# Optimization experiments

Measured on AMD Instinct MI355X. Metric: run time of the kernel, lower is better.

Reference implementation:

```python
import jax, jax.numpy as jnp
import numpy as np

D, DFFN, H, P, L = 256, 1024, 8, 4, 4
B, LQ = 32, 300
LENS = [2048, 1024, 512, 256]
STARTS = [0, 2048, 3072, 3584]
S = sum(LENS)


def setup_inputs() -> dict:
    key = jax.random.key(0)
    ks = iter(jax.random.split(key, 64))
    def W(shape, s=0.02):
        return jax.random.normal(next(ks), shape, jnp.float32) * s
    inp = {}
    inp['tgt'] = W((B, LQ, D), 1.0)
    inp['query_pos'] = W((B, LQ, D), 1.0)
    centers = jax.random.uniform(next(ks), (B, LQ, L))
    widths = 0.05 + 0.2 * jax.random.uniform(next(ks), (B, LQ, L))
    inp['reference_points'] = jnp.stack([centers, widths], -1)  # (B,Lq,L,2) = (center,width)
    inp['src'] = W((B, S, D), 1.0)
    inp['temporal_lengths'] = np.array(LENS, np.int64)
    inp['level_start_index'] = np.array(STARTS, np.int64)
    for n, shape in [('sa_qw', (D, D)), ('sa_kw', (D, D)), ('sa_vw', (D, D)), ('sa_ow', (D, D)), ('ff1_w', (D, DFFN)), ('ff2_w', (DFFN, D))]:
        inp[n] = W(shape)
    for n, sz in [('sa_qb', D), ('sa_kb', D), ('sa_vb', D), ('sa_ob', D), ('ff1_b', DFFN), ('ff2_b', D)]:
        inp[n] = jnp.zeros((sz,), jnp.float32)
    for pre in ['ca', 'se']:
        inp[pre + '_off_w'] = W((D, H * L * P))
        inp[pre + '_off_b'] = jnp.zeros((H * L * P,), jnp.float32)
        inp[pre + '_attn_w'] = W((D, H * L * P))
        inp[pre + '_attn_b'] = jnp.zeros((H * L * P,), jnp.float32)
        inp[pre + '_val_w'] = W((D, D))
        inp[pre + '_val_b'] = jnp.zeros((D,), jnp.float32)
        inp[pre + '_out_w'] = W((D, D))
        inp[pre + '_out_b'] = jnp.zeros((D,), jnp.float32)
    for n in ['ln1', 'lnse', 'ln2', 'ln3']:
        inp[n + '_g'] = jnp.ones((D,), jnp.float32)
        inp[n + '_b'] = jnp.zeros((D,), jnp.float32)
    return inp


def _ln(x, g, b, eps=1e-5):
    m = jnp.mean(x, -1, keepdims=True)
    v = jnp.mean((x - m) ** 2, -1, keepdims=True)
    return (x - m) * jax.lax.rsqrt(v + eps) * g + b


def _mha(q, k, v, qw, qb, kw, kb, vw, vb, ow, ob):
    b, lq, d = q.shape
    dh = d // H
    qh = (q @ qw + qb).reshape(b, lq, H, dh).transpose(0, 2, 1, 3)
    kh = (k @ kw + kb).reshape(b, -1, H, dh).transpose(0, 2, 1, 3)
    vh = (v @ vw + vb).reshape(b, -1, H, dh).transpose(0, 2, 1, 3)
    scores = jnp.einsum('bhqd,bhkd->bhqk', qh, kh) * (dh ** -0.5)
    attn = jax.nn.softmax(scores, -1)
    out = jnp.einsum('bhqk,bhkd->bhqd', attn, vh).transpose(0, 2, 1, 3).reshape(b, lq, d)
    return out @ ow + ob


def _deform(q, ref, src, lens, starts, vw, vb, offw, offb, aw, ab, ow, ob, boundary):
    b, lq, d = q.shape
    dh = d // H
    value = (src @ vw + vb).reshape(b, -1, H, dh)  # (B,S,H,Dh)
    off = (q @ offw + offb).reshape(b, lq, H, L, P)
    attn = jax.nn.softmax((q @ aw + ab).reshape(b, lq, H, L * P), -1).reshape(b, lq, H, L, P)
    center = ref[..., 0][:, :, None, :, None]  # (B,Lq,1,L,1)
    width = ref[..., 1][:, :, None, :, None]
    if boundary:
        # half the points anchored at segment start, half at segment end
        sign = jnp.where(jnp.arange(P) < P // 2, -0.5, 0.5)
        anchor = center + sign * width
    else:
        anchor = center
    loc = anchor + off / P * width * 0.5  # normalized sampling locations (B,Lq,H,L,P)
    out = jnp.zeros((b, lq, H, dh), value.dtype)
    for l in range(L):
        T = int(lens[l]); s0 = int(starts[l])
        v = value[:, s0:s0 + T].transpose(0, 2, 1, 3)  # (B,H,T,Dh)
        x = loc[:, :, :, l, :] * T - 0.5  # align_corners=False grid
        x0 = jnp.floor(x)
        w = x - x0
        i0 = x0.astype(jnp.int32)
        i1 = i0 + 1
        m0 = ((i0 >= 0) & (i0 < T)).astype(v.dtype)
        m1 = ((i1 >= 0) & (i1 < T)).astype(v.dtype)
        i0c = jnp.clip(i0, 0, T - 1)
        i1c = jnp.clip(i1, 0, T - 1)
        def gather(idx):
            idxh = idx.transpose(0, 2, 1, 3).reshape(b, H, lq * P, 1)
            g = jnp.take_along_axis(v, jnp.broadcast_to(idxh, (b, H, lq * P, dh)), axis=2)
            return g.reshape(b, H, lq, P, dh).transpose(0, 2, 1, 3, 4)  # (B,Lq,H,P,Dh)
        samp = gather(i0c) * ((1 - w) * m0)[..., None] + gather(i1c) * (w * m1)[..., None]
        out = out + jnp.einsum('bqhp,bqhpd->bqhd', attn[:, :, :, l, :], samp)
    return out.reshape(b, lq, d) @ ow + ob


def reference(tgt, query_pos, reference_points, src, temporal_lengths, level_start_index,
              sa_qw, sa_qb, sa_kw, sa_kb, sa_vw, sa_vb, sa_ow, sa_ob,
              ca_off_w, ca_off_b, ca_attn_w, ca_attn_b, ca_val_w, ca_val_b, ca_out_w, ca_out_b,
              se_off_w, se_off_b, se_attn_w, se_attn_b, se_val_w, se_val_b, se_out_w, se_out_b,
              ff1_w, ff1_b, ff2_w, ff2_b,
              ln1_g, ln1_b, lnse_g, lnse_b, ln2_g, ln2_b, ln3_g, ln3_b):
    lens = np.asarray(temporal_lengths)
    starts = np.asarray(level_start_index)
    q = tgt + query_pos
    t2 = _mha(q, q, tgt, sa_qw, sa_qb, sa_kw, sa_kb, sa_vw, sa_vb, sa_ow, sa_ob)
    tgt = _ln(tgt + t2, ln2_g, ln2_b)
    t2 = _deform(tgt + query_pos, reference_points, src, lens, starts,
                 ca_val_w, ca_val_b, ca_off_w, ca_off_b, ca_attn_w, ca_attn_b, ca_out_w, ca_out_b, False)
    tgt = _ln(tgt + t2, ln1_g, ln1_b)
    t2 = _deform(tgt + query_pos, reference_points, src, lens, starts,
                 se_val_w, se_val_b, se_off_w, se_off_b, se_attn_w, se_attn_b, se_out_w, se_out_b, True)
    tgt = _ln(tgt + t2, lnse_g, lnse_b)
    t2 = jax.nn.relu(tgt @ ff1_w + ff1_b) @ ff2_w + ff2_b
    tgt = _ln(tgt + t2, ln3_g, ln3_b)
    return tgt
```

## Files before the change

kernel.cpp:

```cpp
#include <hip/hip_runtime.h>
#include <hip/hip_bf16.h>

namespace {

typedef unsigned short u16;
typedef unsigned int u32;

constexpr int D    = 256;
constexpr int H    = 8;
constexpr int DH   = 32;
constexpr int B    = 32;
constexpr int LQ   = 300;
constexpr int NQ   = B * LQ;
constexpr int S    = 3840;
constexpr int MS   = B * S;
constexpr int DFFN = 1024;

typedef __attribute__((ext_vector_type(8))) short bf16x8;
typedef __attribute__((ext_vector_type(4))) float f32x4;

__device__ inline u16 f2b(float x) {
  u32 u = __builtin_bit_cast(u32, x);
  u32 r = (u + 0x7FFFu + ((u >> 16) & 1u)) >> 16;
  return (u16)r;
}
__device__ inline u32 pk2(float a, float b) {
  return (u32)f2b(a) | ((u32)f2b(b) << 16);
}
__device__ inline void unpack2(u32 w, float& a, float& b) {
  a = __builtin_bit_cast(float, w << 16);
  b = __builtin_bit_cast(float, w & 0xffff0000u);
}

__global__ __launch_bounds__(256) void gemm_qkv(
    const u16* __restrict__ qbuf, const u16* __restrict__ tgtb,
    const u16* __restrict__ saqk_t, const u16* __restrict__ sav_t,
    const float* __restrict__ qkb, const float* __restrict__ vbias,
    u16* __restrict__ qkbuf, u16* __restrict__ vh)
{
  constexpr int K = 256, BK = 64, LDK = 72;
  __shared__ __align__(16) u16 sh[128 * LDK];
  u16* As = sh;
  u16* Bs = sh + 64 * LDK;
  const bool isv = blockIdx.x >= 8;
  const u16* A  = isv ? tgtb : qbuf;
  const u16* Bt = isv ? sav_t : saqk_t;
  const float* bias = isv ? vbias : qkb;
  u16* C = isv ? vh : qkbuf;
  const int N = isv ? 256 : 512;
  const int n0 = (isv ? (int)blockIdx.x - 8 : (int)blockIdx.x) * 64;
  const int m0 = blockIdx.y * 64;

  const int tid  = threadIdx.x;
  const int lane = tid & 63;
  const int wid  = tid >> 6;
  const int wm = wid >> 1, wn = wid & 1;

  f32x4 acc[2][2] = {};
  uint4 ra[2], rb[2];
  const int srow = tid >> 3, sch = (tid & 7) * 8;

#pragma unroll
  for (int i = 0; i < 2; ++i) {
    const int row = srow + i * 32;
    ra[i] = *(const uint4*)(A  + (size_t)(m0 + row) * K + sch);
    rb[i] = *(const uint4*)(Bt + (size_t)(n0 + row) * K + sch);
  }
  for (int t = 0; t < 4; ++t) {
#pragma unroll
    for (int i = 0; i < 2; ++i) {
      const int row = srow + i * 32;
      *(uint4*)(&As[row * LDK + sch]) = ra[i];
      *(uint4*)(&Bs[row * LDK + sch]) = rb[i];
    }
    __syncthreads();
    if (t + 1 < 4) {
      const int k0 = (t + 1) * BK;
#pragma unroll
      for (int i = 0; i < 2; ++i) {
        const int row = srow + i * 32;
        ra[i] = *(const uint4*)(A  + (size_t)(m0 + row) * K + k0 + sch);
        rb[i] = *(const uint4*)(Bt + (size_t)(n0 + row) * K + k0 + sch);
      }
    }
#pragma unroll
    for (int kk = 0; kk < 2; ++kk) {
      const int krd = kk * 32 + (lane >> 4) * 8;
      bf16x8 af[2], bf[2];
#pragma unroll
      for (int m = 0; m < 2; ++m)
        af[m] = *(const bf16x8*)(&As[(wm * 32 + (lane & 15) + 16 * m) * LDK + krd]);
#pragma unroll
      for (int n = 0; n < 2; ++n)
        bf[n] = *(const bf16x8*)(&Bs[(wn * 32 + (lane & 15) + 16 * n) * LDK + krd]);
#pragma unroll
      for (int m = 0; m < 2; ++m)
#pragma unroll
        for (int n = 0; n < 2; ++n)
          acc[m][n] = __builtin_amdgcn_mfma_f32_16x16x32_bf16(af[m], bf[n], acc[m][n], 0, 0, 0);
    }
    __syncthreads();
  }

  const int cr = (lane >> 4) * 4;
  const int cc = lane & 15;
  u16* stg = sh;
#pragma unroll
  for (int n = 0; n < 2; ++n) {
    const int lc = wn * 32 + n * 16 + cc;
    const float bv = bias[n0 + lc];
#pragma unroll
    for (int m = 0; m < 2; ++m) {
      const int lr0 = wm * 32 + m * 16 + cr;
#pragma unroll
      for (int r = 0; r < 4; ++r)
        stg[(lr0 + r) * LDK + lc] = f2b(acc[m][n][r] + bv);
    }
  }
  __syncthreads();
#pragma unroll
  for (int i = 0; i < 2; ++i) {
    const int c = tid + 256 * i;
    const int row = c >> 3, ch = c & 7;
    *(uint4*)(C + (size_t)(m0 + row) * N + n0 + ch * 8) =
        *(const uint4*)(&stg[row * LDK + ch * 8]);
  }
}

__global__ __launch_bounds__(512) void gemm_val4(
    const float* __restrict__ A, const u16* __restrict__ Bt2,
    const float* __restrict__ bias2, u16* __restrict__ Vca, u16* __restrict__ Vse)
{
  __shared__ __align__(16) char shraw[33792];
  char* Asw = shraw;
  const int tid  = threadIdx.x;
  const int lane = tid & 63;
  const int w    = tid >> 6;
  const int bid  = blockIdx.x;
  const int nh   = (bid >> 3) & 1;
  const int m0   = ((bid >> 4) * 8 + (bid & 7)) * 64;
  u16* dst = nh ? Vse : Vca;
  const u16* Bt = Bt2 + nh * 256 * 256;
  const float* bias = bias2 + nh * 256;
  const int b  = m0 / S;
  const int s0 = m0 - b * S;

#pragma unroll
  for (int i = 0; i < 4; ++i) {
    const int idx = tid + 512 * i;
    const int row = idx >> 5, ch = idx & 31;
    const float* ap = A + (size_t)(m0 + row) * 256 + ch * 8;
    const float4 f0 = *(const float4*)(ap);
    const float4 f1 = *(const float4*)(ap + 4);
    uint4 pk;
    pk.x = pk2(f0.x, f0.y); pk.y = pk2(f0.z, f0.w);
    pk.z = pk2(f1.x, f1.y); pk.w = pk2(f1.z, f1.w);
    *(uint4*)(Asw + row * 512 + ((ch * 16) ^ ((row & 7) << 4))) = pk;
  }
  __syncthreads();

  f32x4 acc[4][2] = {};
  const u16* bb = Bt + (size_t)(w * 32 + (lane & 15)) * 256 + (lane >> 4) * 8;
  bf16x8 bcur[2], bnxt[2];
#pragma unroll
  for (int n = 0; n < 2; ++n) bcur[n] = *(const bf16x8*)(bb + n * 4096);

#pragma unroll
  for (int kk = 0; kk < 8; ++kk) {
    bf16x8 af[4];
    const int kb = kk * 64 + (lane >> 4) * 16;
#pragma unroll
    for (int m = 0; m < 4; ++m) {
      const int row = m * 16 + (lane & 15);
      af[m] = *(const bf16x8*)(Asw + row * 512 + (kb ^ ((row & 7) << 4)));
    }
    if (kk < 7) {
#pragma unroll
      for (int n = 0; n < 2; ++n)
        bnxt[n] = *(const bf16x8*)(bb + n * 4096 + (kk + 1) * 32);
    }
#pragma unroll
    for (int m = 0; m < 4; ++m)
#pragma unroll
      for (int n = 0; n < 2; ++n)
        acc[m][n] = __builtin_amdgcn_mfma_f32_16x16x32_bf16(af[m], bcur[n], acc[m][n], 0, 0, 0);
#pragma unroll
    for (int n = 0; n < 2; ++n) bcur[n] = bnxt[n];
  }
  __syncthreads();

  constexpr int STC = 264;
  u16* stg = (u16*)shraw;
  const int cr = (lane >> 4) * 4;
  const int cc = lane & 15;
#pragma unroll
  for (int n = 0; n < 2; ++n) {
    const int col = w * 32 + n * 16 + cc;
    const float bv = bias[col];
#pragma unroll
    for (int m = 0; m < 4; ++m) {
      const int r0 = m * 16 + cr;
#pragma unroll
      for (int r = 0; r < 4; ++r)
        stg[(r0 + r) * STC + col] = f2b(acc[m][n][r] + bv);
    }
  }
  __syncthreads();
  u16* vb = dst + (size_t)b * H * S * DH;
#pragma unroll
  for (int i = 0; i < 4; ++i) {
    const int c = tid + 512 * i;
    const int row = c >> 5, ch = c & 31;
    const int h = ch >> 2, dq = ch & 3;
    *(uint4*)(vb + ((size_t)h * S + (s0 + row)) * DH + dq * 8) =
        *(const uint4*)(&stg[row * STC + ch * 8]);
  }
}

__global__ __launch_bounds__(1024) void gemm_lnoff(
    const u16* __restrict__ A, const u16* __restrict__ Bt,
    const float* __restrict__ bias, const float* __restrict__ res,
    const float* __restrict__ g, const float* __restrict__ be,
    const float* __restrict__ qpos,
    const u16* __restrict__ offw, const float* __restrict__ offb,
    float* __restrict__ fout, float* __restrict__ oaout)
{
  constexpr int K = 256, LDK = 72;
  __shared__ __align__(16) float ftile[64 * 264];
  u16* As = (u16*)ftile;
  u16* Bs = As + 64 * LDK;
  u16* aq = (u16*)ftile;
  const int tid  = threadIdx.x;
  const int lane = tid & 63;
  const int wid  = tid >> 6;
  const int wm = wid >> 2, wn = wid & 3;
  const int m0 = blockIdx.x * 64;

  f32x4 acc[4] = {};
  const bool am = tid < 512;
  const int arow = tid >> 3, ach = (tid & 7) * 8;

  uint4 ra = {};
  uint4 rb[2];
  if (am) ra = *(const uint4*)(A + (size_t)(m0 + arow) * K + ach);
#pragma unroll
  for (int i = 0; i < 2; ++i) {
    const int idx = tid + 1024 * i;
    const int brow = idx >> 3, bch = (idx & 7) * 8;
    rb[i] = *(const uint4*)(Bt + (size_t)brow * K + bch);
  }

  for (int t = 0; t < 4; ++t) {
    if (am) *(uint4*)(&As[arow * LDK + ach]) = ra;
#pragma unroll
    for (int i = 0; i < 2; ++i) {
      const int idx = tid + 1024 * i;
      const int brow = idx >> 3, bch = (idx & 7) * 8;
      *(uint4*)(&Bs[brow * LDK + bch]) = rb[i];
    }
    __syncthreads();
    if (t + 1 < 4) {
      const int k0 = (t + 1) * 64;
      if (am) ra = *(const uint4*)(A + (size_t)(m0 + arow) * K + k0 + ach);
#pragma unroll
      for (int i = 0; i < 2; ++i) {
        const int idx = tid + 1024 * i;
        const int brow = idx >> 3, bch = (idx & 7) * 8;
        rb[i] = *(const uint4*)(Bt + (size_t)brow * K + k0 + bch);
      }
    }
#pragma unroll
    for (int kk = 0; kk < 2; ++kk) {
      const int krd = kk * 32 + (lane >> 4) * 8;
      bf16x8 af, bf[4];
      af = *(const bf16x8*)(&As[(wm * 16 + (lane & 15)) * LDK + krd]);
#pragma unroll
      for (int n = 0; n < 4; ++n)
        bf[n] = *(const bf16x8*)(&Bs[(wn * 64 + n * 16 + (lane & 15)) * LDK + krd]);
#pragma unroll
      for (int n = 0; n < 4; ++n)
        acc[n] = __builtin_amdgcn_mfma_f32_16x16x32_bf16(af, bf[n], acc[n], 0, 0, 0);
    }
    __syncthreads();
  }

  const int cr = (lane >> 4) * 4;
  const int cc = lane & 15;
#pragma unroll
  for (int n = 0; n < 4; ++n) {
    const int col = wn * 64 + n * 16 + cc;
    const float bv = bias[col];
#pragma unroll
    for (int r = 0; r < 4; ++r)
      ftile[(wm * 16 + cr + r) * 264 + col] = acc[n][r] + bv;
  }
  __syncthreads();

  const int row = tid >> 4, s16 = tid & 15;
  const size_t grow = (size_t)(m0 + row) * 256;
  float vv[16];
  float sum = 0.f;
#pragma unroll
  for (int j = 0; j < 4; ++j) {
    const int col = s16 * 4 + j * 64;
    const float4 fv = *(const float4*)(&ftile[row * 264 + col]);
    const float4 rv = *(const float4*)(res + grow + col);
    vv[j * 4 + 0] = fv.x + rv.x; vv[j * 4 + 1] = fv.y + rv.y;
    vv[j * 4 + 2] = fv.z + rv.z; vv[j * 4 + 3] = fv.w + rv.w;
    sum += vv[j * 4 + 0] + vv[j * 4 + 1] + vv[j * 4 + 2] + vv[j * 4 + 3];
  }
  sum += __shfl_xor(sum, 1, 64);
  sum += __shfl_xor(sum, 2, 64);
  sum += __shfl_xor(sum, 4, 64);
  sum += __shfl_xor(sum, 8, 64);
  const float mean = sum * (1.f / 256.f);
  float sq = 0.f;
#pragma unroll
  for (int k = 0; k < 16; ++k) { const float d = vv[k] - mean; sq += d * d; }
  sq += __shfl_xor(sq, 1, 64);
  sq += __shfl_xor(sq, 2, 64);
  sq += __shfl_xor(sq, 4, 64);
  sq += __shfl_xor(sq, 8, 64);
  const float rstd = rsqrtf(sq * (1.f / 256.f) + 1e-5f);

  float yq[16];
#pragma unroll
  for (int j = 0; j < 4; ++j) {
    const int col = s16 * 4 + j * 64;
    const float4 gv = *(const float4*)(g + col);
    const float4 bv = *(const float4*)(be + col);
    const float4 qv = *(const float4*)(qpos + grow + col);
    float4 y;
    y.x = (vv[j * 4 + 0] - mean) * rstd * gv.x + bv.x;
    y.y = (vv[j * 4 + 1] - mean) * rstd * gv.y + bv.y;
    y.z = (vv[j * 4 + 2] - mean) * rstd * gv.z + bv.z;
    y.w = (vv[j * 4 + 3] - mean) * rstd * gv.w + bv.w;
    *(float4*)(fout + grow + col) = y;
    yq[j * 4 + 0] = y.x + qv.x; yq[j * 4 + 1] = y.y + qv.y;
    yq[j * 4 + 2] = y.z + qv.z; yq[j * 4 + 3] = y.w + qv.w;
  }
  __syncthreads();

#pragma unroll
  for (int j = 0; j < 4; ++j) {
    const int col = s16 * 4 + j * 64;
    uint2 pk;
    pk.x = pk2(yq[j * 4 + 0], yq[j * 4 + 1]);
    pk.y = pk2(yq[j * 4 + 2], yq[j * 4 + 3]);
    *(uint2*)(&aq[row * 264 + col]) = pk;
  }
  __syncthreads();

  f32x4 acc2[4] = {};
  const u16* bb = offw + (size_t)(wn * 64 + (lane & 15)) * 256 + (lane >> 4) * 8;
#pragma unroll
  for (int kk = 0; kk < 8; ++kk) {
    const bf16x8 af = *(const bf16x8*)(&aq[(wm * 16 + (lane & 15)) * 264 + kk * 32 + (lane >> 4) * 8]);
#pragma unroll
    for (int n = 0; n < 4; ++n) {
      const bf16x8 bf = *(const bf16x8*)(bb + (size_t)n * 16 * 256 + kk * 32);
      acc2[n] = __builtin_amdgcn_mfma_f32_16x16x32_bf16(af, bf, acc2[n], 0, 0, 0);
    }
  }
  __syncthreads();

#pragma unroll
  for (int n = 0; n < 4; ++n) {
    const int col = wn * 64 + n * 16 + cc;
    const float bv = offb[col];
#pragma unroll
    for (int r = 0; r < 4; ++r)
      ftile[(wm * 16 + cr + r) * 264 + col] = acc2[n][r] + bv;
  }
  __syncthreads();
#pragma unroll
  for (int i = 0; i < 4; ++i) {
    const int c = tid + 1024 * i;
    const int rw = c >> 6, ch = c & 63;
    *(float4*)(oaout + (size_t)(m0 + rw) * 256 + ch * 4) =
        *(const float4*)(&ftile[rw * 264 + ch * 4]);
  }
}

__global__ __launch_bounds__(512) void gemm_tail(
    const u16* __restrict__ A, const u16* __restrict__ Wout,
    const float* __restrict__ bout, const float* __restrict__ res,
    const float* __restrict__ g1, const float* __restrict__ be1,
    const u16* __restrict__ B1t, const u16* __restrict__ B2t,
    const float* __restrict__ b1, const float* __restrict__ b2,
    const float* __restrict__ g2, const float* __restrict__ be2,
    float* __restrict__ fout)
{
  __shared__ __align__(16) char sh[81920];
  char* Ast = sh;
  char* ffh = sh + 16384;
  float* ftile = (float*)sh;
  const int tid  = threadIdx.x;
  const int lane = tid & 63;
  const int w    = tid >> 6;
  const int m0   = blockIdx.x * 32;
  const int cr = (lane >> 4) * 4;
  const int cc = lane & 15;

#pragma unroll
  for (int i = 0; i < 2; ++i) {
    const int idx = tid + 512 * i;
    const int row = idx >> 5, ch = idx & 31;
    const uint4 v = *(const uint4*)(A + (size_t)(m0 + row) * 256 + ch * 8);
    *(uint4*)(Ast + row * 512 + ((ch * 16) ^ ((row & 7) << 4))) = v;
  }
  __syncthreads();

  f32x4 accB[2][2] = {};
  {
    const u16* bb = Wout + (size_t)(w * 32 + (lane & 15)) * 256 + (lane >> 4) * 8;
#pragma unroll
    for (int kk = 0; kk < 8; ++kk) {
      bf16x8 af[2];
      const int kb = kk * 64 + (lane >> 4) * 16;
#pragma unroll
      for (int m = 0; m < 2; ++m) {
        const int row = m * 16 + (lane & 15);
        af[m] = *(const bf16x8*)(Ast + row * 512 + (kb ^ ((row & 7) << 4)));
      }
#pragma unroll
      for (int n = 0; n < 2; ++n) {
        const bf16x8 bf = *(const bf16x8*)(bb + (size_t)n * 16 * 256 + kk * 32);
#pragma unroll
        for (int m = 0; m < 2; ++m)
          accB[m][n] = __builtin_amdgcn_mfma_f32_16x16x32_bf16(af[m], bf, accB[m][n], 0, 0, 0);
      }
    }
  }
  __syncthreads();

#pragma unroll
  for (int n = 0; n < 2; ++n) {
    const int col = w * 32 + n * 16 + cc;
    const float bv = bout[col];
#pragma unroll
    for (int m = 0; m < 2; ++m)
#pragma unroll
      for (int r = 0; r < 4; ++r)
        ftile[(m * 16 + cr + r) * 264 + col] = accB[m][n][r] + bv;
  }
  __syncthreads();

  const int row = tid >> 4, s16 = tid & 15;
  const size_t grow = (size_t)(m0 + row) * 256;
  float yv[16];
  {
    float vv[16];
    float sum = 0.f;
#pragma unroll
    for (int j = 0; j < 4; ++j) {
      const int col = s16 * 4 + j * 64;
      const float4 fv = *(const float4*)(&ftile[row * 264 + col]);
      const float4 rv = *(const float4*)(res + grow + col);
      vv[j * 4 + 0] = fv.x + rv.x; vv[j * 4 + 1] = fv.y + rv.y;
      vv[j * 4 + 2] = fv.z + rv.z; vv[j * 4 + 3] = fv.w + rv.w;
      sum += vv[j * 4 + 0] + vv[j * 4 + 1] + vv[j * 4 + 2] + vv[j * 4 + 3];
    }
    sum += __shfl_xor(sum, 1, 64);
    sum += __shfl_xor(sum, 2, 64);
    sum += __shfl_xor(sum, 4, 64);
    sum += __shfl_xor(sum, 8, 64);
    const float mean = sum * (1.f / 256.f);
    float sq = 0.f;
#pragma unroll
    for (int k = 0; k < 16; ++k) { const float d = vv[k] - mean; sq += d * d; }
    sq += __shfl_xor(sq, 1, 64);
    sq += __shfl_xor(sq, 2, 64);
    sq += __shfl_xor(sq, 4, 64);
    sq += __shfl_xor(sq, 8, 64);
    const float rstd = rsqrtf(sq * (1.f / 256.f) + 1e-5f);
#pragma unroll
    for (int j = 0; j < 4; ++j) {
      const int col = s16 * 4 + j * 64;
      const float4 gv = *(const float4*)(g1 + col);
      const float4 bv = *(const float4*)(be1 + col);
      yv[j * 4 + 0] = (vv[j * 4 + 0] - mean) * rstd * gv.x + bv.x;
      yv[j * 4 + 1] = (vv[j * 4 + 1] - mean) * rstd * gv.y + bv.y;
      yv[j * 4 + 2] = (vv[j * 4 + 2] - mean) * rstd * gv.z + bv.z;
      yv[j * 4 + 3] = (vv[j * 4 + 3] - mean) * rstd * gv.w + bv.w;
    }
  }
  __syncthreads();

#pragma unroll
  for (int j = 0; j < 4; ++j) {
    const int col = s16 * 4 + j * 64;
    uint2 pk;
    pk.x = pk2(yv[j * 4 + 0], yv[j * 4 + 1]);
    pk.y = pk2(yv[j * 4 + 2], yv[j * 4 + 3]);
    *(uint2*)(Ast + row * 512 + ((col * 2) ^ ((row & 7) << 4))) = pk;
  }
  __syncthreads();

  {
    f32x4 acc[2][8] = {};
    const u16* bb = B1t + (size_t)(w * 128 + (lane & 15)) * 256 + (lane >> 4) * 8;
#pragma unroll
    for (int kk = 0; kk < 8; ++kk) {
      bf16x8 af[2];
      const int kb = kk * 64 + (lane >> 4) * 16;
#pragma unroll
      for (int m = 0; m < 2; ++m) {
        const int rw = m * 16 + (lane & 15);
        af[m] = *(const bf16x8*)(Ast + rw * 512 + (kb ^ ((rw & 7) << 4)));
      }
#pragma unroll
      for (int n = 0; n < 8; ++n) {
        const bf16x8 bf = *(const bf16x8*)(bb + (size_t)n * 16 * 256 + kk * 32);
#pragma unroll
        for (int m = 0; m < 2; ++m)
          acc[m][n] = __builtin_amdgcn_mfma_f32_16x16x32_bf16(af[m], bf, acc[m][n], 0, 0, 0);
      }
    }
#pragma unroll
    for (int n = 0; n < 8; ++n) {
      const int col = w * 128 + n * 16 + cc;
      const float bv = b1[col];
#pragma unroll
      for (int m = 0; m < 2; ++m) {
#pragma unroll
        for (int r = 0; r < 4; ++r) {
          const int rw = m * 16 + cr + r;
          const float x = fmaxf(acc[m][n][r] + bv, 0.f);
          *(u16*)(ffh + rw * 2048 + ((col * 2) ^ ((rw & 7) << 4))) = f2b(x);
        }
      }
    }
  }
  __syncthreads();

  f32x4 acc2[2][2] = {};
  {
    const u16* bb = B2t + (size_t)(w * 32 + (lane & 15)) * 1024 + (lane >> 4) * 8;
#pragma unroll 4
    for (int kk = 0; kk < 32; ++kk) {
      bf16x8 af[2];
      const int kb = kk * 64 + (lane >> 4) * 16;
#pragma unroll
      for (int m = 0; m < 2; ++m) {
        const int rw = m * 16 + (lane & 15);
        af[m] = *(const bf16x8*)(ffh + rw * 2048 + (kb ^ ((rw & 7) << 4)));
      }
#pragma unroll
      for (int n = 0; n < 2; ++n) {
        const bf16x8 bf = *(const bf16x8*)(bb + (size_t)n * 16 * 1024 + kk * 32);
#pragma unroll
        for (int m = 0; m < 2; ++m)
          acc2[m][n] = __builtin_amdgcn_mfma_f32_16x16x32_bf16(af[m], bf, acc2[m][n], 0, 0, 0);
      }
    }
  }
  __syncthreads();

#pragma unroll
  for (int n = 0; n < 2; ++n) {
    const int col = w * 32 + n * 16 + cc;
    const float bv = b2[col];
#pragma unroll
    for (int m = 0; m < 2; ++m)
#pragma unroll
      for (int r = 0; r < 4; ++r)
        ftile[(m * 16 + cr + r) * 264 + col] = acc2[m][n][r] + bv;
  }
  __syncthreads();

  {
    float vv[16];
    float sum = 0.f;
#pragma unroll
    for (int j = 0; j < 4; ++j) {
      const int col = s16 * 4 + j * 64;
      const float4 fv = *(const float4*)(&ftile[row * 264 + col]);
      vv[j * 4 + 0] = fv.x + yv[j * 4 + 0]; vv[j * 4 + 1] = fv.y + yv[j * 4 + 1];
      vv[j * 4 + 2] = fv.z + yv[j * 4 + 2]; vv[j * 4 + 3] = fv.w + yv[j * 4 + 3];
      sum += vv[j * 4 + 0] + vv[j * 4 + 1] + vv[j * 4 + 2] + vv[j * 4 + 3];
    }
    sum += __shfl_xor(sum, 1, 64);
    sum += __shfl_xor(sum, 2, 64);
    sum += __shfl_xor(sum, 4, 64);
    sum += __shfl_xor(sum, 8, 64);
    const float mean = sum * (1.f / 256.f);
    float sq = 0.f;
#pragma unroll
    for (int k = 0; k < 16; ++k) { const float d = vv[k] - mean; sq += d * d; }
    sq += __shfl_xor(sq, 1, 64);
    sq += __shfl_xor(sq, 2, 64);
    sq += __shfl_xor(sq, 4, 64);
    sq += __shfl_xor(sq, 8, 64);
    const float rstd = rsqrtf(sq * (1.f / 256.f) + 1e-5f);
#pragma unroll
    for (int j = 0; j < 4; ++j) {
      const int col = s16 * 4 + j * 64;
      const float4 gv = *(const float4*)(g2 + col);
      const float4 bv = *(const float4*)(be2 + col);
      float4 y;
      y.x = (vv[j * 4 + 0] - mean) * rstd * gv.x + bv.x;
      y.y = (vv[j * 4 + 1] - mean) * rstd * gv.y + bv.y;
      y.z = (vv[j * 4 + 2] - mean) * rstd * gv.z + bv.z;
      y.w = (vv[j * 4 + 3] - mean) * rstd * gv.w + bv.w;
      *(float4*)(fout + grow + col) = y;
    }
  }
}

struct WSpec { const float* w; u16* wt; int K, N, blk0; };
struct WPack { WSpec s[14]; };

struct PrepArgs {
  const float *ca_off_b, *ca_attn_b, *se_off_b, *se_attn_b;
  const float *sa_qb, *sa_kb, *ca_val_b, *se_val_b;
  float *bias4, *qkb, *valb;
  const float *tgt, *qpos;
  u16 *tgtb, *qbuf;
  int n4, nwt;
};

__global__ __launch_bounds__(256) void prep_all(WPack p, PrepArgs a) {
  __shared__ float tile[32][33];
  const int b = blockIdx.x;
  if (b < a.nwt) {
    int i = 0;
#pragma unroll
    for (int j = 1; j < 14; ++j) if (b >= p.s[j].blk0) i = j;
    const float* w = p.s[i].w;
    u16* wt = p.s[i].wt;
    const int K = p.s[i].K, N = p.s[i].N;
    const int lb = b - p.s[i].blk0;
    const int ntN = N >> 5;
    const int tk = lb / ntN, tn = lb - tk * ntN;
    const int r = threadIdx.x >> 5, c = threadIdx.x & 31;
#pragma unroll
    for (int j = 0; j < 4; ++j)
      tile[r + j * 8][c] = w[(size_t)(tk * 32 + r + j * 8) * N + tn * 32 + c];
    __syncthreads();
#pragma unroll
    for (int j = 0; j < 4; ++j)
      wt[(size_t)(tn * 32 + r + j * 8) * K + tk * 32 + c] = f2b(tile[c][r + j * 8]);
  } else if (b == a.nwt) {
#pragma unroll
    for (int u = 0; u < 2; ++u) {
      const int t = threadIdx.x + 256 * u;
      a.bias4[t] = t < 128 ? a.ca_off_b[t] : t < 256 ? a.ca_attn_b[t - 128]
                 : t < 384 ? a.se_off_b[t - 256] : a.se_attn_b[t - 384];
      a.qkb[t]  = t < 256 ? a.sa_qb[t] : a.sa_kb[t - 256];
      a.valb[t] = t < 256 ? a.ca_val_b[t] : a.se_val_b[t - 256];
    }
  } else {
    const int i = (b - a.nwt - 1) * 256 + threadIdx.x;
    if (i < a.n4) {
      const float4 t = ((const float4*)a.tgt)[i];
      const float4 q = ((const float4*)a.qpos)[i];
      uint2 x, y;
      x.x = pk2(t.x, t.y); x.y = pk2(t.z, t.w);
      y.x = pk2(t.x + q.x, t.y + q.y); y.y = pk2(t.z + q.z, t.w + q.w);
      ((uint2*)a.tgtb)[i] = x;
      ((uint2*)a.qbuf)[i] = y;
    }
  }
}

__global__ __launch_bounds__(512) void mha_v2(
    const u16* __restrict__ qk, const u16* __restrict__ vh,
    u16* __restrict__ out)
{
  __shared__ __align__(16) float Ks[8 * 300 * 4];
  __shared__ __align__(16) float Vs[8 * 300 * 4];
  const int bh  = blockIdx.x & 255;
  const int seg = blockIdx.x >> 8;
  const int b = bh >> 3, h = bh & 7;
  const u16* kbase = qk + (size_t)b * LQ * 512 + 256 + h * DH;
  const u16* vbase = vh + (size_t)b * LQ * D + h * DH;
  for (int e = threadIdx.x; e < 300 * 8; e += 512) {
    const int r = e >> 3, j = e & 7;
    float4 f;
    const uint2 kv = *(const uint2*)(kbase + (size_t)r * 512 + j * 4);
    unpack2(kv.x, f.x, f.y);
    unpack2(kv.y, f.z, f.w);
    *(float4*)(&Ks[(j * 300 + r) * 4]) = f;
    const uint2 vv = *(const uint2*)(vbase + (size_t)r * D + j * 4);
    unpack2(vv.x, f.x, f.y);
    unpack2(vv.y, f.z, f.w);
    *(float4*)(&Vs[(j * 300 + r) * 4]) = f;
  }
  __syncthreads();

  const int lane = threadIdx.x & 63;
  const int lq = (threadIdx.x >> 6) * 16 + (lane >> 2);
  const int kc = lane & 3;
  const int q = seg * 128 + lq;
  if (q >= LQ) return;

  const u16* qrow = qk + (size_t)(b * LQ + q) * 512 + h * DH;
  float qv[DH];
#pragma unroll
  for (int c4 = 0; c4 < 4; ++c4) {
    const uint4 u = *(const uint4*)(qrow + c4 * 8);
    unpack2(u.x, qv[c4 * 8 + 0], qv[c4 * 8 + 1]);
    unpack2(u.y, qv[c4 * 8 + 2], qv[c4 * 8 + 3]);
    unpack2(u.z, qv[c4 * 8 + 4], qv[c4 * 8 + 5]);
    unpack2(u.w, qv[c4 * 8 + 6], qv[c4 * 8 + 7]);
  }
#pragma unroll
  for (int d = 0; d < DH; ++d) qv[d] *= 0.17677669529663689f;

  float o[DH] = {};
  float ssum = 0.f;
  const float* kp = &Ks[kc * 75 * 4];
  const float* vp = &Vs[kc * 75 * 4];
  for (int i = 0; i < 75; ++i) {
    float s = 0.f;
#pragma unroll
    for (int j = 0; j < 8; ++j) {
      const float4 kf = *(const float4*)(kp + i * 4 + j * 1200);
      s += qv[j * 4 + 0] * kf.x + qv[j * 4 + 1] * kf.y
         + qv[j * 4 + 2] * kf.z + qv[j * 4 + 3] * kf.w;
    }
    const float p = __expf(s);
    ssum += p;
#pragma unroll
    for (int j = 0; j < 8; ++j) {
      const float4 vf = *(const float4*)(vp + i * 4 + j * 1200);
      o[j * 4 + 0] += p * vf.x; o[j * 4 + 1] += p * vf.y;
      o[j * 4 + 2] += p * vf.z; o[j * 4 + 3] += p * vf.w;
    }
  }

  ssum += __shfl_xor(ssum, 1, 64);
  ssum += __shfl_xor(ssum, 2, 64);
#pragma unroll
  for (int d = 0; d < DH; ++d) {
    o[d] += __shfl_xor(o[d], 1, 64);
    o[d] += __shfl_xor(o[d], 2, 64);
  }
  const float inv = 1.f / ssum;

  u16* orow = out + (size_t)(b * LQ + q) * D + h * DH;
#pragma unroll
  for (int c = 0; c < 4; ++c) {
    if (kc == c) {
      uint4 w;
      w.x = pk2(o[c * 8 + 0] * inv, o[c * 8 + 1] * inv);
      w.y = pk2(o[c * 8 + 2] * inv, o[c * 8 + 3] * inv);
      w.z = pk2(o[c * 8 + 4] * inv, o[c * 8 + 5] * inv);
      w.w = pk2(o[c * 8 + 6] * inv, o[c * 8 + 7] * inv);
      *(uint4*)(orow + c * 8) = w;
    }
  }
}

template<bool BOUNDARY>
__global__ __launch_bounds__(512) void deform_v4(
    const float* __restrict__ oa, const float* __restrict__ ref,
    const u16* __restrict__ value, u16* __restrict__ out)
{
  __shared__ __align__(16) uint4 owt[4][128];
  const int unit = threadIdx.x >> 7;
  const int bq = blockIdx.x * 4 + unit;
  const int b = bq / LQ;
  const int t = threadIdx.x & 127;
  const int h = t >> 4;
  const int l = (t >> 2) & 3;
  const int p = t & 3;

  const float off   = oa[(size_t)bq * 256 + t];
  const float logit = oa[(size_t)bq * 256 + 128 + t];
  const float center = ref[(size_t)bq * 8 + l * 2 + 0];
  const float width  = ref[(size_t)bq * 8 + l * 2 + 1];

  const float e = __expf(logit);
  float ssum = e;
  ssum += __shfl_xor(ssum, 1, 64);
  ssum += __shfl_xor(ssum, 2, 64);
  ssum += __shfl_xor(ssum, 4, 64);
  ssum += __shfl_xor(ssum, 8, 64);
  const float wa = e / ssum;

  const int T  = 2048 >> l;
  const int s0 = 4096 - (4096 >> l);
  float anchor = center;
  if (BOUNDARY) anchor += (p < 2 ? -0.5f : 0.5f) * width;
  const float loc = anchor + off * width * 0.125f;
  const float x = loc * (float)T - 0.5f;
  const float x0 = floorf(x);
  const float w = x - x0;
  const int i0 = (int)x0;
  const int i1 = i0 + 1;
  const float w0 = (i0 >= 0 && i0 < T) ? wa * (1.f - w) : 0.f;
  const float w1 = (i1 >= 0 && i1 < T) ? wa * w : 0.f;
  const int i0c = min(max(i0, 0), T - 1);
  const int i1c = min(max(i1, 0), T - 1);
  uint4 pack;
  pack.x = (u32)((h * S + s0 + i0c) * (DH * 2));
  pack.y = __builtin_bit_cast(u32, w0);
  pack.z = (u32)((h * S + s0 + i1c) * (DH * 2));
  pack.w = __builtin_bit_cast(u32, w1);
  owt[unit][t] = pack;
  __syncthreads();

  const int g  = t >> 4;
  const int ln = t & 15;
  const int qd = ln & 3;
  const int ts = ln >> 2;
  const char* vb = (const char*)(value + (size_t)b * H * S * DH) + qd * 16;
  float o[8] = {};
#pragma unroll
  for (int i = 0; i < 8; ++i) {
    const int rowidx = i * 4 + ts;
    const uint4 ow = owt[unit][g * 16 + (rowidx >> 1)];
    const u32 boff = (rowidx & 1) ? ow.z : ow.x;
    const float wt = __builtin_bit_cast(float, (rowidx & 1) ? ow.w : ow.y);
    const uint4 v = *(const uint4*)(vb + boff);
    float a0, a1;
    unpack2(v.x, a0, a1); o[0] += wt * a0; o[1] += wt * a1;
    unpack2(v.y, a0, a1); o[2] += wt * a0; o[3] += wt * a1;
    unpack2(v.z, a0, a1); o[4] += wt * a0; o[5] += wt * a1;
    unpack2(v.w, a0, a1); o[6] += wt * a0; o[7] += wt * a1;
  }
#pragma unroll
  for (int d = 0; d < 8; ++d) {
    o[d] += __shfl_xor(o[d], 4, 64);
    o[d] += __shfl_xor(o[d], 8, 64);
  }
  if (ts == 0) {
    uint4 wv;
    wv.x = pk2(o[0], o[1]); wv.y = pk2(o[2], o[3]);
    wv.z = pk2(o[4], o[5]); wv.w = pk2(o[6], o[7]);
    *(uint4*)(out + (size_t)bq * D + g * DH + qd * 8) = wv;
  }
}

}

extern "C" void kernel_launch(void* const* d_in, const int* in_sizes, int n_in,
                              void* d_out, int out_size, void* d_ws, size_t ws_size,
                              hipStream_t stream)
{
  const float* tgt   = (const float*)d_in[0];
  const float* qpos  = (const float*)d_in[1];
  const float* ref   = (const float*)d_in[2];
  const float* src   = (const float*)d_in[3];
  const float* sa_qw = (const float*)d_in[6];
  const float* sa_kw = (const float*)d_in[7];
  const float* sa_vw = (const float*)d_in[8];
  const float* sa_ow = (const float*)d_in[9];
  const float* ff1_w = (const float*)d_in[10];
  const float* ff2_w = (const float*)d_in[11];
  const float* sa_qb = (const float*)d_in[12];
  const float* sa_kb = (const float*)d_in[13];
  const float* sa_vb = (const float*)d_in[14];
  const float* sa_ob = (const float*)d_in[15];
  const float* ff1_b = (const float*)d_in[16];
  const float* ff2_b = (const float*)d_in[17];
  const float* ca_off_w  = (const float*)d_in[18];
  const float* ca_off_b  = (const float*)d_in[19];
  const float* ca_attn_w = (const float*)d_in[20];
  const float* ca_attn_b = (const float*)d_in[21];
  const float* ca_val_w  = (const float*)d_in[22];
  const float* ca_val_b  = (const float*)d_in[23];
  const float* ca_out_w  = (const float*)d_in[24];
  const float* ca_out_b  = (const float*)d_in[25];
  const float* se_off_w  = (const float*)d_in[26];
  const float* se_off_b  = (const float*)d_in[27];
  const float* se_attn_w = (const float*)d_in[28];
  const float* se_attn_b = (const float*)d_in[29];
  const float* se_val_w  = (const float*)d_in[30];
  const float* se_val_b  = (const float*)d_in[31];
  const float* se_out_w  = (const float*)d_in[32];
  const float* se_out_b  = (const float*)d_in[33];
  const float* ln1_g  = (const float*)d_in[34];
  const float* ln1_b  = (const float*)d_in[35];
  const float* lnse_g = (const float*)d_in[36];
  const float* lnse_b = (const float*)d_in[37];
  const float* ln2_g  = (const float*)d_in[38];
  const float* ln2_b  = (const float*)d_in[39];
  const float* ln3_g  = (const float*)d_in[40];
  const float* ln3_b  = (const float*)d_in[41];

  const size_t ND = (size_t)NQ * D;
  const size_t MD = (size_t)MS * D;

  char* base = (char*)d_ws;
  size_t off = 0;
  auto alloc = [&](size_t bytes) -> void* {
    void* p = base + off;
    off += (bytes + 255) & ~(size_t)255;
    return p;
  };
  u16*  Vca  = (u16*)alloc(MD * 2);
  u16*  Vse  = (u16*)alloc(MD * 2);
  u16*  qkbuf = (u16*)alloc((size_t)NQ * 512 * 2);
  u16*  vh   = (u16*)alloc(ND * 2);
  u16*  qbuf = (u16*)alloc(ND * 2);
  u16*  smpb = (u16*)alloc(ND * 2);
  u16*  tgtb = (u16*)alloc(ND * 2);
  float* cur = (float*)alloc(ND * 4);
  float* oabuf = (float*)alloc((size_t)NQ * 256 * 4);
  float* bias4 = (float*)alloc(512 * 4);
  float* qkb   = (float*)alloc(512 * 4);
  float* valb  = (float*)alloc(512 * 4);

  WPack pk;
  int wi = 0, blk = 0;
  auto addw = [&](const float* w, int K, int N) -> u16* {
    u16* wt = (u16*)alloc((size_t)K * N * 2);
    pk.s[wi].w = w; pk.s[wi].wt = wt; pk.s[wi].K = K; pk.s[wi].N = N; pk.s[wi].blk0 = blk;
    blk += (K / 32) * (N / 32);
    ++wi;
    return wt;
  };
  u16* saq_t = addw(sa_qw, D, D);
  u16* sak_t = addw(sa_kw, D, D);        (void)sak_t;
  u16* sav_t = addw(sa_vw, D, D);
  u16* sao_t = addw(sa_ow, D, D);
  u16* ff1_t = addw(ff1_w, D, DFFN);
  u16* ff2_t = addw(ff2_w, DFFN, D);
  u16* caoff_t = addw(ca_off_w, D, 128);
  u16* caatt_t = addw(ca_attn_w, D, 128);  (void)caatt_t;
  u16* seoff_t = addw(se_off_w, D, 128);
  u16* seatt_t = addw(se_attn_w, D, 128);  (void)seatt_t;
  u16* caval_t = addw(ca_val_w, D, D);
  u16* seval_t = addw(se_val_w, D, D);     (void)seval_t;
  u16* caout_t = addw(ca_out_w, D, D);
  u16* seout_t = addw(se_out_w, D, D);

  const int n4 = (int)(ND / 4);

  PrepArgs pa;
  pa.ca_off_b = ca_off_b; pa.ca_attn_b = ca_attn_b;
  pa.se_off_b = se_off_b; pa.se_attn_b = se_attn_b;
  pa.sa_qb = sa_qb; pa.sa_kb = sa_kb; pa.ca_val_b = ca_val_b; pa.se_val_b = se_val_b;
  pa.bias4 = bias4; pa.qkb = qkb; pa.valb = valb;
  pa.tgt = tgt; pa.qpos = qpos; pa.tgtb = tgtb; pa.qbuf = qbuf;
  pa.n4 = n4; pa.nwt = blk;
  prep_all<<<blk + 1 + 2400, 256, 0, stream>>>(pk, pa);

  gemm_val4<<<(MS / 64) * 2, 512, 0, stream>>>(src, caval_t, valb, Vca, Vse);

  gemm_qkv<<<dim3(12, 150), 256, 0, stream>>>(qbuf, tgtb, saq_t, sav_t, qkb, sa_vb, qkbuf, vh);
  mha_v2<<<B * H * 3, 512, 0, stream>>>(qkbuf, vh, smpb);
  gemm_lnoff<<<NQ / 64, 1024, 0, stream>>>(smpb, sao_t, sa_ob, tgt, ln2_g, ln2_b,
                                           qpos, caoff_t, bias4, cur, oabuf);

  deform_v4<false><<<NQ / 4, 512, 0, stream>>>(oabuf, ref, Vca, smpb);
  gemm_lnoff<<<NQ / 64, 1024, 0, stream>>>(smpb, caout_t, ca_out_b, cur, ln1_g, ln1_b,
                                           qpos, seoff_t, bias4 + 256, cur, oabuf);

  deform_v4<true><<<NQ / 4, 512, 0, stream>>>(oabuf, ref, Vse, smpb);

  gemm_tail<<<NQ / 32, 512, 0, stream>>>(smpb, seout_t, se_out_b, cur,
                                         lnse_g, lnse_b, ff1_t, ff2_t,
                                         ff1_b, ff2_b, ln3_g, ln3_b,
                                         (float*)d_out);
}
```

Baseline: 422.5 us.

## Fuse deformable sampling into the following out-proj/LayerNorm GEMM kernels

Removes the standalone deform_v4 kernels. The sampling now runs as a prologue phase inside the output-projection kernels: deform_lnoff handles the cross-attention path and gemm_tail2 the boundary path. Each 32-query block computes its offsets and weights into shared memory, gathers bilinear samples, and writes the bf16 result straight into the swizzled A tile. This cuts two launches and the global round-trip of the sampled activations. In exchange the gathers run in only 300 blocks of 512 threads with about 80KB of shared memory each, so there is less parallelism to hide gather latency.

After: 416.5 us, median of 2. About the same (-1.4%).

```diff
diff --git a/kernel.cpp b/kernel.cpp
--- a/kernel.cpp
+++ b/kernel.cpp
@@ -30,6 +30,98 @@
 __device__ inline void unpack2(u32 w, float& a, float& b) {
   a = __builtin_bit_cast(float, w << 16);
   b = __builtin_bit_cast(float, w & 0xffff0000u);
+}
+
+template<bool BOUNDARY>
+__device__ inline void deform_phase(
+    int tid, int m0,
+    const float* __restrict__ oa, const float* __restrict__ ref,
+    const u16* __restrict__ value, uint4* owt , char* Ast)
+{
+#pragma unroll
+  for (int qq = 0; qq < 8; ++qq) {
+    const int ql = (tid >> 7) + 4 * qq;
+    const int bq = m0 + ql;
+    const int t  = tid & 127;
+    const int h = t >> 4;
+    const int l = (t >> 2) & 3;
+    const int p = t & 3;
+
+    const float off    = oa[(size_t)bq * 256 + t];
+    const float logit  = oa[(size_t)bq * 256 + 128 + t];
+    const float center = ref[(size_t)bq * 8 + l * 2 + 0];
+    const float width  = ref[(size_t)bq * 8 + l * 2 + 1];
+
+    const float e = __expf(logit);
+    float ssum = e;
+    ssum += __shfl_xor(ssum, 1, 64);
+    ssum += __shfl_xor(ssum, 2, 64);
+    ssum += __shfl_xor(ssum, 4, 64);
+    ssum += __shfl_xor(ssum, 8, 64);
+    const float wa = e / ssum;
+
+    const int T  = 2048 >> l;
+    const int s0 = 4096 - (4096 >> l);
+    float anchor = center;
+    if (BOUNDARY) anchor += (p < 2 ? -0.5f : 0.5f) * width;
+    const float loc = anchor + off * width * 0.125f;
+    const float x = loc * (float)T - 0.5f;
+    const float x0 = floorf(x);
+    const float w = x - x0;
+    const int i0 = (int)x0;
+    const int i1 = i0 + 1;
+    const float w0 = (i0 >= 0 && i0 < T) ? wa * (1.f - w) : 0.f;
+    const float w1 = (i1 >= 0 && i1 < T) ? wa * w : 0.f;
+    const int i0c = min(max(i0, 0), T - 1);
+    const int i1c = min(max(i1, 0), T - 1);
+    uint4 pack;
+    pack.x = (u32)((h * S + s0 + i0c) * (DH * 2));
+    pack.y = __builtin_bit_cast(u32, w0);
+    pack.z = (u32)((h * S + s0 + i1c) * (DH * 2));
+    pack.w = __builtin_bit_cast(u32, w1);
+    owt[ql * 128 + t] = pack;
+  }
+  __syncthreads();
+
+#pragma unroll
+  for (int qq = 0; qq < 8; ++qq) {
+    const int ql = (tid >> 7) + 4 * qq;
+    const int bq = m0 + ql;
+    const int b = bq / LQ;
+    const int t = tid & 127;
+    const int g  = t >> 4;
+    const int ln = t & 15;
+    const int qd = ln & 3;
+    const int ts = ln >> 2;
+    const char* vb = (const char*)(value + (size_t)b * H * S * DH) + qd * 16;
+    float o[8] = {};
+#pragma unroll
+    for (int i = 0; i < 8; ++i) {
+      const int rowidx = i * 4 + ts;
+      const uint4 ow = owt[ql * 128 + g * 16 + (rowidx >> 1)];
+      const u32 boff = (rowidx & 1) ? ow.z : ow.x;
+      const float wt = __builtin_bit_cast(float, (rowidx & 1) ? ow.w : ow.y);
+      const uint4 v = *(const uint4*)(vb + boff);
+      float a0, a1;
+      unpack2(v.x, a0, a1); o[0] += wt * a0; o[1] += wt * a1;
+      unpack2(v.y, a0, a1); o[2] += wt * a0; o[3] += wt * a1;
+      unpack2(v.z, a0, a1); o[4] += wt * a0; o[5] += wt * a1;
+      unpack2(v.w, a0, a1); o[6] += wt * a0; o[7] += wt * a1;
+    }
+#pragma unroll
+    for (int d = 0; d < 8; ++d) {
+      o[d] += __shfl_xor(o[d], 4, 64);
+      o[d] += __shfl_xor(o[d], 8, 64);
+    }
+    if (ts == 0) {
+      const int col = g * DH + qd * 8;
+      uint4 wv;
+      wv.x = pk2(o[0], o[1]); wv.y = pk2(o[2], o[3]);
+      wv.z = pk2(o[4], o[5]); wv.w = pk2(o[6], o[7]);
+      *(uint4*)(Ast + ql * 512 + ((col * 2) ^ ((ql & 7) << 4))) = wv;
+    }
+  }
+  __syncthreads();
 }
 
 __global__ __launch_bounds__(256) void gemm_qkv(
@@ -382,9 +474,165 @@
   }
 }
 
-__global__ __launch_bounds__(512) void gemm_tail(
-    const u16* __restrict__ A, const u16* __restrict__ Wout,
-    const float* __restrict__ bout, const float* __restrict__ res,
+__global__ __launch_bounds__(512) void deform_lnoff(
+    const float* __restrict__ oa, const float* __restrict__ ref,
+    const u16* __restrict__ value,
+    const u16* __restrict__ Wout, const float* __restrict__ bout,
+    const float* __restrict__ res, const float* __restrict__ g,
+    const float* __restrict__ be, const float* __restrict__ qpos,
+    const u16* __restrict__ offw, const float* __restrict__ offb,
+    float* __restrict__ fout, float* __restrict__ oaout)
+{
+  __shared__ __align__(16) char sh[81920];
+  char* Ast = sh;
+  uint4* owt = (uint4*)(sh + 16384);
+  float* ftile = (float*)sh;
+  u16* aq = (u16*)sh;
+  const int tid  = threadIdx.x;
+  const int lane = tid & 63;
+  const int w    = tid >> 6;
+  const int m0   = blockIdx.x * 32;
+  const int cr = (lane >> 4) * 4;
+  const int cc = lane & 15;
+
+  deform_phase<false>(tid, m0, oa, ref, value, owt, Ast);
+
+  f32x4 accB[2][2] = {};
+  {
+    const u16* bb = Wout + (size_t)(w * 32 + (lane & 15)) * 256 + (lane >> 4) * 8;
+#pragma unroll
+    for (int kk = 0; kk < 8; ++kk) {
+      bf16x8 af[2];
+      const int kb = kk * 64 + (lane >> 4) * 16;
+#pragma unroll
+      for (int m = 0; m < 2; ++m) {
+        const int row = m * 16 + (lane & 15);
+        af[m] = *(const bf16x8*)(Ast + row * 512 + (kb ^ ((row & 7) << 4)));
+      }
+#pragma unroll
+      for (int n = 0; n < 2; ++n) {
+        const bf16x8 bf = *(const bf16x8*)(bb + (size_t)n * 16 * 256 + kk * 32);
+#pragma unroll
+        for (int m = 0; m < 2; ++m)
+          accB[m][n] = __builtin_amdgcn_mfma_f32_16x16x32_bf16(af[m], bf, accB[m][n], 0, 0, 0);
+      }
+    }
+  }
+  __syncthreads();
+
+#pragma unroll
+  for (int n = 0; n < 2; ++n) {
+    const int col = w * 32 + n * 16 + cc;
+    const float bv = bout[col];
+#pragma unroll
+    for (int m = 0; m < 2; ++m)
+#pragma unroll
+      for (int r = 0; r < 4; ++r)
+        ftile[(m * 16 + cr + r) * 264 + col] = accB[m][n][r] + bv;
+  }
+  __syncthreads();
+
+  const int row = tid >> 4, s16 = tid & 15;
+  const size_t grow = (size_t)(m0 + row) * 256;
+  float yq[16];
+  {
+    float vv[16];
+    float sum = 0.f;
+#pragma unroll
+    for (int j = 0; j < 4; ++j) {
+      const int col = s16 * 4 + j * 64;
+      const float4 fv = *(const float4*)(&ftile[row * 264 + col]);
+      const float4 rv = *(const float4*)(res + grow + col);
+      vv[j * 4 + 0] = fv.x + rv.x; vv[j * 4 + 1] = fv.y + rv.y;
+      vv[j * 4 + 2] = fv.z + rv.z; vv[j * 4 + 3] = fv.w + rv.w;
+      sum += vv[j * 4 + 0] + vv[j * 4 + 1] + vv[j * 4 + 2] + vv[j * 4 + 3];
+    }
+    sum += __shfl_xor(sum, 1, 64);
+    sum += __shfl_xor(sum, 2, 64);
+    sum += __shfl_xor(sum, 4, 64);
+    sum += __shfl_xor(sum, 8, 64);
+    const float mean = sum * (1.f / 256.f);
+    float sq = 0.f;
+#pragma unroll
+    for (int k = 0; k < 16; ++k) { const float d = vv[k] - mean; sq += d * d; }
+    sq += __shfl_xor(sq, 1, 64);
+    sq += __shfl_xor(sq, 2, 64);
+    sq += __shfl_xor(sq, 4, 64);
+    sq += __shfl_xor(sq, 8, 64);
+    const float rstd = rsqrtf(sq * (1.f / 256.f) + 1e-5f);
+#pragma unroll
+    for (int j = 0; j < 4; ++j) {
+      const int col = s16 * 4 + j * 64;
+      const float4 gv = *(const float4*)(g + col);
+      const float4 bv = *(const float4*)(be + col);
+      const float4 qv = *(const float4*)(qpos + grow + col);
+      float4 y;
+      y.x = (vv[j * 4 + 0] - mean) * rstd * gv.x + bv.x;
+      y.y = (vv[j * 4 + 1] - mean) * rstd * gv.y + bv.y;
+      y.z = (vv[j * 4 + 2] - mean) * rstd * gv.z + bv.z;
+      y.w = (vv[j * 4 + 3] - mean) * rstd * gv.w + bv.w;
+      *(float4*)(fout + grow + col) = y;
+      yq[j * 4 + 0] = y.x + qv.x; yq[j * 4 + 1] = y.y + qv.y;
+      yq[j * 4 + 2] = y.z + qv.z; yq[j * 4 + 3] = y.w + qv.w;
+    }
+  }
+  __syncthreads();
+
+#pragma unroll
+  for (int j = 0; j < 4; ++j) {
+    const int col = s16 * 4 + j * 64;
+    uint2 pk;
+    pk.x = pk2(yq[j * 4 + 0], yq[j * 4 + 1]);
+    pk.y = pk2(yq[j * 4 + 2], yq[j * 4 + 3]);
+    *(uint2*)(&aq[row * 264 + col]) = pk;
+  }
+  __syncthreads();
+
+  f32x4 acc2[2][2] = {};
+  {
+    const u16* bb = offw + (size_t)(w * 32 + (lane & 15)) * 256 + (lane >> 4) * 8;
+#pragma unroll
+    for (int kk = 0; kk < 8; ++kk) {
+      bf16x8 af[2];
+#pragma unroll
+      for (int m = 0; m < 2; ++m)
+        af[m] = *(const bf16x8*)(&aq[(m * 16 + (lane & 15)) * 264 + kk * 32 + (lane >> 4) * 8]);
+#pragma unroll
+      for (int n = 0; n < 2; ++n) {
+        const bf16x8 bf = *(const bf16x8*)(bb + (size_t)n * 16 * 256 + kk * 32);
+#pragma unroll
+        for (int m = 0; m < 2; ++m)
+          acc2[m][n] = __builtin_amdgcn_mfma_f32_16x16x32_bf16(af[m], bf, acc2[m][n], 0, 0, 0);
+      }
+    }
+  }
+  __syncthreads();
+
+#pragma unroll
+  for (int n = 0; n < 2; ++n) {
+    const int col = w * 32 + n * 16 + cc;
+    const float bv = offb[col];
+#pragma unroll
+    for (int m = 0; m < 2; ++m)
+#pragma unroll
+      for (int r = 0; r < 4; ++r)
+        ftile[(m * 16 + cr + r) * 264 + col] = acc2[m][n][r] + bv;
+  }
+  __syncthreads();
+#pragma unroll
+  for (int i = 0; i < 4; ++i) {
+    const int c = tid + 512 * i;
+    const int rw = c >> 6, ch = c & 63;
+    *(float4*)(oaout + (size_t)(m0 + rw) * 256 + ch * 4) =
+        *(const float4*)(&ftile[rw * 264 + ch * 4]);
+  }
+}
+
+__global__ __launch_bounds__(512) void gemm_tail2(
+    const float* __restrict__ oa, const float* __restrict__ ref,
+    const u16* __restrict__ value,
+    const u16* __restrict__ Wout, const float* __restrict__ bout,
+    const float* __restrict__ res,
     const float* __restrict__ g1, const float* __restrict__ be1,
     const u16* __restrict__ B1t, const u16* __restrict__ B2t,
     const float* __restrict__ b1, const float* __restrict__ b2,
@@ -393,6 +641,7 @@
 {
   __shared__ __align__(16) char sh[81920];
   char* Ast = sh;
+  uint4* owt = (uint4*)(sh + 16384);
   char* ffh = sh + 16384;
   float* ftile = (float*)sh;
   const int tid  = threadIdx.x;
@@ -402,14 +651,7 @@
   const int cr = (lane >> 4) * 4;
   const int cc = lane & 15;
 
-#pragma unroll
-  for (int i = 0; i < 2; ++i) {
-    const int idx = tid + 512 * i;
-    const int row = idx >> 5, ch = idx & 31;
-    const uint4 v = *(const uint4*)(A + (size_t)(m0 + row) * 256 + ch * 8);
-    *(uint4*)(Ast + row * 512 + ((ch * 16) ^ ((row & 7) << 4))) = v;
-  }
-  __syncthreads();
+  deform_phase<true>(tid, m0, oa, ref, value, owt, Ast);
 
   f32x4 accB[2][2] = {};
   {
@@ -750,87 +992,6 @@
       w.w = pk2(o[c * 8 + 6] * inv, o[c * 8 + 7] * inv);
       *(uint4*)(orow + c * 8) = w;
     }
-  }
-}
-
-template<bool BOUNDARY>
-__global__ __launch_bounds__(512) void deform_v4(
-    const float* __restrict__ oa, const float* __restrict__ ref,
-    const u16* __restrict__ value, u16* __restrict__ out)
-{
-  __shared__ __align__(16) uint4 owt[4][128];
-  const int unit = threadIdx.x >> 7;
-  const int bq = blockIdx.x * 4 + unit;
-  const int b = bq / LQ;
-  const int t = threadIdx.x & 127;
-  const int h = t >> 4;
-  const int l = (t >> 2) & 3;
-  const int p = t & 3;
-
-  const float off   = oa[(size_t)bq * 256 + t];
-  const float logit = oa[(size_t)bq * 256 + 128 + t];
-  const float center = ref[(size_t)bq * 8 + l * 2 + 0];
-  const float width  = ref[(size_t)bq * 8 + l * 2 + 1];
-
-  const float e = __expf(logit);
-  float ssum = e;
-  ssum += __shfl_xor(ssum, 1, 64);
-  ssum += __shfl_xor(ssum, 2, 64);
-  ssum += __shfl_xor(ssum, 4, 64);
-  ssum += __shfl_xor(ssum, 8, 64);
-  const float wa = e / ssum;
-
-  const int T  = 2048 >> l;
-  const int s0 = 4096 - (4096 >> l);
-  float anchor = center;
-  if (BOUNDARY) anchor += (p < 2 ? -0.5f : 0.5f) * width;
-  const float loc = anchor + off * width * 0.125f;
-  const float x = loc * (float)T - 0.5f;
-  const float x0 = floorf(x);
-  const float w = x - x0;
-  const int i0 = (int)x0;
-  const int i1 = i0 + 1;
-  const float w0 = (i0 >= 0 && i0 < T) ? wa * (1.f - w) : 0.f;
-  const float w1 = (i1 >= 0 && i1 < T) ? wa * w : 0.f;
-  const int i0c = min(max(i0, 0), T - 1);
-  const int i1c = min(max(i1, 0), T - 1);
-  uint4 pack;
-  pack.x = (u32)((h * S + s0 + i0c) * (DH * 2));
-  pack.y = __builtin_bit_cast(u32, w0);
-  pack.z = (u32)((h * S + s0 + i1c) * (DH * 2));
-  pack.w = __builtin_bit_cast(u32, w1);
-  owt[unit][t] = pack;
-  __syncthreads();
-
-  const int g  = t >> 4;
-  const int ln = t & 15;
-  const int qd = ln & 3;
-  const int ts = ln >> 2;
-  const char* vb = (const char*)(value + (size_t)b * H * S * DH) + qd * 16;
-  float o[8] = {};
-#pragma unroll
-  for (int i = 0; i < 8; ++i) {
-    const int rowidx = i * 4 + ts;
-    const uint4 ow = owt[unit][g * 16 + (rowidx >> 1)];
-    const u32 boff = (rowidx & 1) ? ow.z : ow.x;
-    const float wt = __builtin_bit_cast(float, (rowidx & 1) ? ow.w : ow.y);
-    const uint4 v = *(const uint4*)(vb + boff);
-    float a0, a1;
-    unpack2(v.x, a0, a1); o[0] += wt * a0; o[1] += wt * a1;
-    unpack2(v.y, a0, a1); o[2] += wt * a0; o[3] += wt * a1;
-    unpack2(v.z, a0, a1); o[4] += wt * a0; o[5] += wt * a1;
-    unpack2(v.w, a0, a1); o[6] += wt * a0; o[7] += wt * a1;
-  }
-#pragma unroll
-  for (int d = 0; d < 8; ++d) {
-    o[d] += __shfl_xor(o[d], 4, 64);
-    o[d] += __shfl_xor(o[d], 8, 64);
-  }
-  if (ts == 0) {
-    uint4 wv;
-    wv.x = pk2(o[0], o[1]); wv.y = pk2(o[2], o[3]);
-    wv.z = pk2(o[4], o[5]); wv.w = pk2(o[6], o[7]);
-    *(uint4*)(out + (size_t)bq * D + g * DH + qd * 8) = wv;
   }
 }
 
@@ -946,14 +1107,13 @@
   gemm_lnoff<<<NQ / 64, 1024, 0, stream>>>(smpb, sao_t, sa_ob, tgt, ln2_g, ln2_b,
                                            qpos, caoff_t, bias4, cur, oabuf);
 
-  deform_v4<false><<<NQ / 4, 512, 0, stream>>>(oabuf, ref, Vca, smpb);
-  gemm_lnoff<<<NQ / 64, 1024, 0, stream>>>(smpb, caout_t, ca_out_b, cur, ln1_g, ln1_b,
-                                           qpos, seoff_t, bias4 + 256, cur, oabuf);
-
-  deform_v4<true><<<NQ / 4, 512, 0, stream>>>(oabuf, ref, Vse, smpb);
-
-  gemm_tail<<<NQ / 32, 512, 0, stream>>>(smpb, seout_t, se_out_b, cur,
-                                         lnse_g, lnse_b, ff1_t, ff2_t,
-                                         ff1_b, ff2_b, ln3_g, ln3_b,
-                                         (float*)d_out);
-}
+  deform_lnoff<<<NQ / 32, 512, 0, stream>>>(oabuf, ref, Vca,
+                                            caout_t, ca_out_b, cur, ln1_g, ln1_b,
+                                            qpos, seoff_t, bias4 + 256, cur, oabuf);
+
+  gemm_tail2<<<NQ / 32, 512, 0, stream>>>(oabuf, ref, Vse,
+                                          seout_t, se_out_b, cur,
+                                          lnse_g, lnse_b, ff1_t, ff2_t,
+                                          ff1_b, ff2_b, ln3_g, ln3_b,
+                                          (float*)d_out);
+}
```
